# Kernel optimization log

Hardware: AMD Instinct MI355X
Metric: run time of the kernel (lower is better)

Reference implementation:

```python
import jax, jax.numpy as jnp
import numpy as np

N_SRC = 100000
N_DST = 50000
N_EDGES = 1600000
D_IN = 128
D_OUT = 64


def setup_inputs() -> dict:
    key = jax.random.key(0)
    ks = jax.random.split(key, 6)
    x = jax.random.normal(ks[0], (N_SRC, D_IN), dtype=jnp.float32)
    W_l = jax.random.normal(ks[1], (D_IN, D_OUT), dtype=jnp.float32) * (1.0 / np.sqrt(D_IN))
    b_l = jax.random.normal(ks[2], (D_OUT,), dtype=jnp.float32) * 0.01
    W_r = jax.random.normal(ks[3], (D_IN, D_OUT), dtype=jnp.float32) * (1.0 / np.sqrt(D_IN))
    src = jax.random.randint(ks[4], (N_EDGES,), 0, N_SRC, dtype=jnp.int64)
    dst = jax.random.randint(ks[5], (N_EDGES,), 0, N_DST, dtype=jnp.int64)
    edge_index = jnp.stack([src, dst], axis=0)
    return {"x": x, "W_l": W_l, "b_l": b_l, "W_r": W_r,
            "edge_index": edge_index, "n_dst": N_DST}


def reference(x, W_l, b_l, W_r, edge_index, n_dst):
    src, dst = edge_index[0], edge_index[1]
    # gather source features along edges: [E, D_in]
    msgs = x[src]
    # mean aggregation at destination nodes
    agg = jax.ops.segment_sum(msgs, dst, num_segments=n_dst)          # [n_dst, D_in]
    cnt = jax.ops.segment_sum(jnp.ones_like(dst, dtype=x.dtype), dst,
                              num_segments=n_dst)                     # [n_dst]
    mean = agg / jnp.maximum(cnt, 1.0)[:, None]
    x_target = x[:n_dst]
    # SAGEConv: lin_l(mean_agg) + lin_r(x_target)
    out = mean @ W_l + b_l + x_target @ W_r                           # [n_dst, D_out]
    return jax.nn.log_softmax(out, axis=-1)
```

## Files before the change

kernel.cpp:

```cpp
#include <hip/hip_runtime.h>
#include <math.h>

#define DIN  128
#define DOUT 64
#define PROWS 64
#define XPITCH 132
#define BSH  8
#define BMSK 255
#define BCAP 8960

__device__ inline unsigned short f2bf(float f) {
    unsigned u = __float_as_uint(f);
    u += 0x7fffu + ((u >> 16) & 1u);
    return (unsigned short)(u >> 16);
}
__device__ inline float bflo(unsigned u) { return __uint_as_float(u << 16); }
__device__ inline float bfhi(unsigned u) { return __uint_as_float(u & 0xffff0000u); }

__global__ void __launch_bounds__(256) build_k(
    const int* __restrict__ ei, unsigned* __restrict__ gTail,
    int* __restrict__ bucketBuf,
    const float* __restrict__ x, const float* __restrict__ Wl,
    const float* __restrict__ bl, const float* __restrict__ Wr,
    unsigned short* __restrict__ y, float* __restrict__ zout,
    int E, int nFill, int P, int nyb, int n_src, int n_dst, int nB)
{
    __shared__ float s_x[PROWS * XPITCH];
    const int b = blockIdx.x;
    const int fq = b / P;
    const bool isFill = ((b % P) == 0) && (fq < nFill);

    if (isFill) {
        int* s_i  = (int*)s_x;
        int* lcnt = s_i;
        int* lpos = s_i + 256;
        int* s_gb = s_i + 512;
        const int t = threadIdx.x;
        const int myb = (fq * 256 + t) * 8;
        const bool full = (myb + 8 <= E);
        int4 sa, sb4, da, db;
        if (full) {
            sa  = *(const int4*)(ei + myb);
            sb4 = *(const int4*)(ei + myb + 4);
            da  = *(const int4*)(ei + E + myb);
            db  = *(const int4*)(ei + E + myb + 4);
        }
        lcnt[t] = 0; lpos[t] = 0;
        __syncthreads();
        if (full) {
            atomicAdd(&lcnt[da.x >> BSH], 1); atomicAdd(&lcnt[da.y >> BSH], 1);
            atomicAdd(&lcnt[da.z >> BSH], 1); atomicAdd(&lcnt[da.w >> BSH], 1);
            atomicAdd(&lcnt[db.x >> BSH], 1); atomicAdd(&lcnt[db.y >> BSH], 1);
            atomicAdd(&lcnt[db.z >> BSH], 1); atomicAdd(&lcnt[db.w >> BSH], 1);
        } else {
            for (int i = myb; i < E && i < myb + 8; ++i)
                atomicAdd(&lcnt[ei[E + i] >> BSH], 1);
        }
        __syncthreads();
        if (t < nB) s_gb[t] = (int)atomicAdd(&gTail[t], (unsigned)lcnt[t]);
        __syncthreads();
#define PLACE(S, D) { int bk = (D) >> BSH; int p = atomicAdd(&lpos[bk], 1);          \
                      unsigned pos = (unsigned)(s_gb[bk] + p);                        \
                      if (pos < BCAP) bucketBuf[(size_t)bk * BCAP + pos] =            \
                          ((S) << BSH) | ((D) & BMSK); }
        if (full) {
            PLACE(sa.x,  da.x) PLACE(sa.y,  da.y) PLACE(sa.z,  da.z) PLACE(sa.w,  da.w)
            PLACE(sb4.x, db.x) PLACE(sb4.y, db.y) PLACE(sb4.z, db.z) PLACE(sb4.w, db.w)
        } else {
            for (int i = myb; i < E && i < myb + 8; ++i) {
                int s = ei[i], d = ei[E + i];
                PLACE(s, d)
            }
        }
#undef PLACE
        return;
    }

    const int fillsBefore = (fq + 1 < nFill) ? (fq + 1) : nFill;
    const int pb = b - fillsBefore;
    const int t  = threadIdx.x;
    const bool isY = (pb < nyb);
    const int rowBase = (isY ? pb : pb - nyb) * PROWS;
    const int nRows = isY ? n_src : n_dst;
    const float* __restrict__ W = isY ? Wl : Wr;

    {
        const float* xsrc = x + (size_t)rowBase * DIN;
        #pragma unroll
        for (int j = 0; j < 8; ++j) {
            int fi  = t + 256 * j;
            int row = fi >> 5, c4 = fi & 31;
            if (rowBase + row < nRows) {
                float4 v = *(const float4*)(xsrc + (size_t)fi * 4);
                *(float4*)(&s_x[row * XPITCH + c4 * 4]) = v;
            }
        }
    }
    __syncthreads();

    const int cg = t & 15;
    const int rg = t >> 4;
    const int r0 = rg * 4;
    const float* wp = W + cg * 4;

    float4 acc0 = {0.f,0.f,0.f,0.f};
    float4 acc1 = {0.f,0.f,0.f,0.f};
    float4 acc2 = {0.f,0.f,0.f,0.f};
    float4 acc3 = {0.f,0.f,0.f,0.f};

#define ROWFMA(acc, xv)                                                                     \
    acc.x = fmaf(xv.w, w3.x, fmaf(xv.z, w2.x, fmaf(xv.y, w1.x, fmaf(xv.x, w0.x, acc.x)))); \
    acc.y = fmaf(xv.w, w3.y, fmaf(xv.z, w2.y, fmaf(xv.y, w1.y, fmaf(xv.x, w0.y, acc.y)))); \
    acc.z = fmaf(xv.w, w3.z, fmaf(xv.z, w2.z, fmaf(xv.y, w1.z, fmaf(xv.x, w0.z, acc.z)))); \
    acc.w = fmaf(xv.w, w3.w, fmaf(xv.z, w2.w, fmaf(xv.y, w1.w, fmaf(xv.x, w0.w, acc.w))));

    #pragma unroll 2
    for (int k = 0; k < DIN; k += 4) {
        float4 w0 = *(const float4*)(wp + (size_t)(k + 0) * DOUT);
        float4 w1 = *(const float4*)(wp + (size_t)(k + 1) * DOUT);
        float4 w2 = *(const float4*)(wp + (size_t)(k + 2) * DOUT);
        float4 w3 = *(const float4*)(wp + (size_t)(k + 3) * DOUT);
        float4 x0 = *(const float4*)(&s_x[(r0 + 0) * XPITCH + k]);
        float4 x1 = *(const float4*)(&s_x[(r0 + 1) * XPITCH + k]);
        float4 x2 = *(const float4*)(&s_x[(r0 + 2) * XPITCH + k]);
        float4 x3 = *(const float4*)(&s_x[(r0 + 3) * XPITCH + k]);
        ROWFMA(acc0, x0)
        ROWFMA(acc1, x1)
        ROWFMA(acc2, x2)
        ROWFMA(acc3, x3)
    }
#undef ROWFMA

    if (isY) {
        float4 av[4] = {acc0, acc1, acc2, acc3};
        #pragma unroll
        for (int r = 0; r < 4; ++r) {
            int row = rowBase + r0 + r;
            if (row < nRows) {
                uint2 pk;
                pk.x = (unsigned)f2bf(av[r].x) | ((unsigned)f2bf(av[r].y) << 16);
                pk.y = (unsigned)f2bf(av[r].z) | ((unsigned)f2bf(av[r].w) << 16);
                *(uint2*)(y + (size_t)row * DOUT + cg * 4) = pk;
            }
        }
    } else {
        const float4 bv = *(const float4*)(bl + cg * 4);
        float4 av[4] = {acc0, acc1, acc2, acc3};
        #pragma unroll
        for (int r = 0; r < 4; ++r) {
            int row = rowBase + r0 + r;
            if (row < nRows) {
                float4 o;
                o.x = av[r].x + bv.x; o.y = av[r].y + bv.y;
                o.z = av[r].z + bv.z; o.w = av[r].w + bv.w;
                *(float4*)(zout + (size_t)row * DOUT + cg * 4) = o;
            }
        }
    }
}

__global__ void __launch_bounds__(256) bucket_k(
    const unsigned* __restrict__ gTail, const int* __restrict__ bucketBuf,
    int* __restrict__ rs, int* __restrict__ csr, int n_dst, int nB)
{
    __shared__ int s_ent[BCAP];
    __shared__ int s_hist[256];
    __shared__ int s_ofs[256];
    __shared__ int s_part[64];
    __shared__ int s_tails[256];
    __shared__ int s_bstart;
    const int b = blockIdx.x, t = threadIdx.x;
    const int lane = t & 63, wave = t >> 6;

    s_tails[t] = (t < nB) ? (int)gTail[t] : 0;
    s_hist[t] = 0;
    __syncthreads();
    if (t == 0) {
        int acc = 0;
        for (int j = 0; j < b; ++j) {
            int v = s_tails[j];
            acc += (v < BCAP) ? v : BCAP;
        }
        s_bstart = acc;
    }
    int m = s_tails[b]; if (m > BCAP) m = BCAP;
    __syncthreads();

    const int* bb = bucketBuf + (size_t)b * BCAP;
    for (int i = t; i < m; i += 256) {
        int e = bb[i];
        s_ent[i] = e;
        atomicAdd(&s_hist[e & BMSK], 1);
    }
    __syncthreads();

    if (t < 64) {
        s_part[t] = s_hist[4*t] + s_hist[4*t+1] + s_hist[4*t+2] + s_hist[4*t+3];
    }
    __syncthreads();
    if (wave == 0) {
        int v = s_part[lane];
        for (int o = 1; o < 64; o <<= 1) {
            int u = __shfl_up(v, o);
            if (lane >= o) v += u;
        }
        s_part[lane] = v;
    }
    __syncthreads();
    if (t < 64) {
        int base = (t == 0) ? 0 : s_part[t-1];
        int h0 = s_hist[4*t], h1 = s_hist[4*t+1], h2 = s_hist[4*t+2];
        s_ofs[4*t]   = base;
        s_ofs[4*t+1] = base + h0;
        s_ofs[4*t+2] = base + h0 + h1;
        s_ofs[4*t+3] = base + h0 + h1 + h2;
    }
    __syncthreads();

    const int dbase = b << BSH;
    int nloc = n_dst - dbase; if (nloc > 256) nloc = 256;
    const int bstart = s_bstart;
    if (t < nloc) rs[dbase + t] = bstart + s_ofs[t];
    if (t == 0)   rs[dbase + nloc] = bstart + m;
    __syncthreads();

    for (int i = t; i < m; i += 256) {
        int e = s_ent[i];
        int p = atomicAdd(&s_ofs[e & BMSK], 1);
        csr[bstart + p] = e >> BSH;
    }
}

__global__ void __launch_bounds__(256) gather_k(
    const unsigned short* __restrict__ y,
    const int* __restrict__ rs, const int* __restrict__ csr,
    float* __restrict__ out, int n_dst)
{
    const int wave = threadIdx.x >> 6, lane = threadIdx.x & 63;
    const int row = blockIdx.x * 4 + wave;
    if (row >= n_dst) return;

    const int start = rs[row];
    const int deg = rs[row + 1] - start;
    const int g = lane >> 4;
    const int qi = (lane & 15) * 2;
    const int q  = (lane & 15) * 4;
    const unsigned* yw = (const unsigned*)y;

    float4 ac0 = make_float4(0.f,0.f,0.f,0.f);
    float4 ac1 = make_float4(0.f,0.f,0.f,0.f);
    float4 ac2 = make_float4(0.f,0.f,0.f,0.f);
    float4 ac3 = make_float4(0.f,0.f,0.f,0.f);
    const int* srow = csr + start;

    for (int co = 0; co < deg; co += 64) {
        int rem = deg - co; if (rem > 64) rem = 64;
        int idx = (lane < rem) ? srow[co + lane] : 0;
        for (int i = 0; i < rem; i += 16) {
            int e0 = i + g, e1 = i + 4 + g, e2 = i + 8 + g, e3 = i + 12 + g;
            int s0 = __shfl(idx, e0), s1 = __shfl(idx, e1);
            int s2 = __shfl(idx, e2), s3 = __shfl(idx, e3);
            if (e0 < rem) { uint2 u = *(const uint2*)(yw + (size_t)s0 * 32 + qi);
                ac0.x += bflo(u.x); ac0.y += bfhi(u.x);
                ac0.z += bflo(u.y); ac0.w += bfhi(u.y); }
            if (e1 < rem) { uint2 u = *(const uint2*)(yw + (size_t)s1 * 32 + qi);
                ac1.x += bflo(u.x); ac1.y += bfhi(u.x);
                ac1.z += bflo(u.y); ac1.w += bfhi(u.y); }
            if (e2 < rem) { uint2 u = *(const uint2*)(yw + (size_t)s2 * 32 + qi);
                ac2.x += bflo(u.x); ac2.y += bfhi(u.x);
                ac2.z += bflo(u.y); ac2.w += bfhi(u.y); }
            if (e3 < rem) { uint2 u = *(const uint2*)(yw + (size_t)s3 * 32 + qi);
                ac3.x += bflo(u.x); ac3.y += bfhi(u.x);
                ac3.z += bflo(u.y); ac3.w += bfhi(u.y); }
        }
    }
    float4 acc;
    acc.x = (ac0.x + ac1.x) + (ac2.x + ac3.x);
    acc.y = (ac0.y + ac1.y) + (ac2.y + ac3.y);
    acc.z = (ac0.z + ac1.z) + (ac2.z + ac3.z);
    acc.w = (ac0.w + ac1.w) + (ac2.w + ac3.w);

    acc.x += __shfl_xor(acc.x, 32); acc.y += __shfl_xor(acc.y, 32);
    acc.z += __shfl_xor(acc.z, 32); acc.w += __shfl_xor(acc.w, 32);
    acc.x += __shfl_xor(acc.x, 16); acc.y += __shfl_xor(acc.y, 16);
    acc.z += __shfl_xor(acc.z, 16); acc.w += __shfl_xor(acc.w, 16);

    const float scale = 1.0f / (float)(deg > 0 ? deg : 1);
    const float4 zv = *(const float4*)(out + (size_t)row * DOUT + q);
    float4 v;
    v.x = acc.x * scale + zv.x;
    v.y = acc.y * scale + zv.y;
    v.z = acc.z * scale + zv.z;
    v.w = acc.w * scale + zv.w;

    float m = fmaxf(fmaxf(v.x, v.y), fmaxf(v.z, v.w));
    for (int o = 8; o >= 1; o >>= 1) m = fmaxf(m, __shfl_xor(m, o));
    float s = expf(v.x - m) + expf(v.y - m) + expf(v.z - m) + expf(v.w - m);
    for (int o = 8; o >= 1; o >>= 1) s += __shfl_xor(s, o);
    const float lse = m + logf(s);

    if (lane < 16) {
        float4 o4;
        o4.x = v.x - lse; o4.y = v.y - lse; o4.z = v.z - lse; o4.w = v.w - lse;
        *(float4*)(out + (size_t)row * DOUT + q) = o4;
    }
}

extern "C" void kernel_launch(void* const* d_in, const int* in_sizes, int n_in,
                              void* d_out, int out_size, void* d_ws, size_t ws_size,
                              hipStream_t stream)
{
    const float* x  = (const float*)d_in[0];
    const float* Wl = (const float*)d_in[1];
    const float* bl = (const float*)d_in[2];
    const float* Wr = (const float*)d_in[3];
    const int*   ei = (const int*)d_in[4];

    const int E     = in_sizes[4] / 2;
    const int n_src = in_sizes[0] / DIN;
    const int n_dst = out_size / DOUT;
    const int nB    = (n_dst + (1 << BSH) - 1) >> BSH;

    unsigned* gTail = (unsigned*)d_ws;
    int* rs  = (int*)d_ws + 256;
    int* csr = rs + (n_dst + 64);
    int* bucketBuf = csr + E;
    unsigned short* yb = (unsigned short*)(bucketBuf + (size_t)nB * BCAP);

    hipMemsetAsync(gTail, 0, 256 * sizeof(unsigned), stream);

    int nFill = (E + 2047) / 2048;
    int nyb = (n_src + PROWS - 1) / PROWS;
    int nzb = (n_dst + PROWS - 1) / PROWS;
    int total = nFill + nyb + nzb;
    int P = (total + nFill - 1) / nFill;

    build_k<<<total, 256, 0, stream>>>(
        ei, gTail, bucketBuf, x, Wl, bl, Wr, yb, (float*)d_out,
        E, nFill, P, nyb, n_src, n_dst, nB);

    bucket_k<<<nB, 256, 0, stream>>>(gTail, bucketBuf, rs, csr, n_dst, nB);

    int gG = (n_dst + 3) / 4;
    gather_k<<<gG, 256, 0, stream>>>(yb, rs, csr, (float*)d_out, n_dst);
}
```

Baseline: 225.5 us.

## Process three projection tiles per block with register-prefetched next tile

Each projection block in build_k now handles three consecutive 64-row tiles instead of one. It loads the next tile of x into registers while computing the current one, then writes those registers to shared memory between barriers. The aim is to hide global-load latency and cut block launch overhead. The cost is more registers per thread (eight float4 prefetch registers), which may lower occupancy, and fewer blocks to spread across CUs.

```diff
diff --git a/kernel.cpp b/kernel.cpp
--- a/kernel.cpp
+++ b/kernel.cpp
@@ -5,6 +5,7 @@
 #define DOUT 64
 #define PROWS 64
 #define XPITCH 132
+#define NTP  3
 #define BSH  8
 #define BMSK 255
 #define BCAP 8960
@@ -79,34 +80,63 @@
     const int fillsBefore = (fq + 1 < nFill) ? (fq + 1) : nFill;
     const int pb = b - fillsBefore;
     const int t  = threadIdx.x;
-    const bool isY = (pb < nyb);
-    const int rowBase = (isY ? pb : pb - nyb) * PROWS;
-    const int nRows = isY ? n_src : n_dst;
-    const float* __restrict__ W = isY ? Wl : Wr;
-
-    {
-        const float* xsrc = x + (size_t)rowBase * DIN;
-        #pragma unroll
-        for (int j = 0; j < 8; ++j) {
-            int fi  = t + 256 * j;
-            int row = fi >> 5, c4 = fi & 31;
-            if (rowBase + row < nRows) {
-                float4 v = *(const float4*)(xsrc + (size_t)fi * 4);
-                *(float4*)(&s_x[row * XPITCH + c4 * 4]) = v;
-            }
-        }
-    }
-    __syncthreads();
+    const int nzb = (n_dst + PROWS - 1) / PROWS;
+    const int nTiles = nyb + nzb;
+    int tt = pb * NTP;
+    if (tt >= nTiles) return;
 
     const int cg = t & 15;
     const int rg = t >> 4;
     const int r0 = rg * 4;
-    const float* wp = W + cg * 4;
-
-    float4 acc0 = {0.f,0.f,0.f,0.f};
-    float4 acc1 = {0.f,0.f,0.f,0.f};
-    float4 acc2 = {0.f,0.f,0.f,0.f};
-    float4 acc3 = {0.f,0.f,0.f,0.f};
+
+    float4 pf[8];
+    {
+        const bool isY0 = tt < nyb;
+        const int rb = (isY0 ? tt : tt - nyb) * PROWS;
+        const int nR = isY0 ? n_src : n_dst;
+        const float* xsrc = x + (size_t)rb * DIN;
+        #pragma unroll
+        for (int j = 0; j < 8; ++j) {
+            int fi = t + 256 * j;
+            int row = fi >> 5;
+            pf[j] = (rb + row < nR) ? *(const float4*)(xsrc + (size_t)fi * 4)
+                                    : make_float4(0.f, 0.f, 0.f, 0.f);
+        }
+    }
+    #pragma unroll
+    for (int j = 0; j < 8; ++j) {
+        int fi = t + 256 * j, row = fi >> 5, c4 = fi & 31;
+        *(float4*)(&s_x[row * XPITCH + c4 * 4]) = pf[j];
+    }
+    __syncthreads();
+
+    for (int i = 0; i < NTP; ++i) {
+        const int tn = tt + 1;
+        const bool hasNext = (i + 1 < NTP) && (tn < nTiles);
+        if (hasNext) {
+            const bool isYn = tn < nyb;
+            const int rb = (isYn ? tn : tn - nyb) * PROWS;
+            const int nR = isYn ? n_src : n_dst;
+            const float* xsrc = x + (size_t)rb * DIN;
+            #pragma unroll
+            for (int j = 0; j < 8; ++j) {
+                int fi = t + 256 * j;
+                int row = fi >> 5;
+                pf[j] = (rb + row < nR) ? *(const float4*)(xsrc + (size_t)fi * 4)
+                                        : make_float4(0.f, 0.f, 0.f, 0.f);
+            }
+        }
+
+        const bool isY = tt < nyb;
+        const int rowBase = (isY ? tt : tt - nyb) * PROWS;
+        const int nRows = isY ? n_src : n_dst;
+        const float* __restrict__ W = isY ? Wl : Wr;
+        const float* wp = W + cg * 4;
+
+        float4 acc0 = {0.f,0.f,0.f,0.f};
+        float4 acc1 = {0.f,0.f,0.f,0.f};
+        float4 acc2 = {0.f,0.f,0.f,0.f};
+        float4 acc3 = {0.f,0.f,0.f,0.f};
 
 #define ROWFMA(acc, xv)                                                                     \
     acc.x = fmaf(xv.w, w3.x, fmaf(xv.z, w2.x, fmaf(xv.y, w1.x, fmaf(xv.x, w0.x, acc.x)))); \
@@ -114,48 +144,59 @@
     acc.z = fmaf(xv.w, w3.z, fmaf(xv.z, w2.z, fmaf(xv.y, w1.z, fmaf(xv.x, w0.z, acc.z)))); \
     acc.w = fmaf(xv.w, w3.w, fmaf(xv.z, w2.w, fmaf(xv.y, w1.w, fmaf(xv.x, w0.w, acc.w))));
 
-    #pragma unroll 2
-    for (int k = 0; k < DIN; k += 4) {
-        float4 w0 = *(const float4*)(wp + (size_t)(k + 0) * DOUT);
-        float4 w1 = *(const float4*)(wp + (size_t)(k + 1) * DOUT);
-        float4 w2 = *(const float4*)(wp + (size_t)(k + 2) * DOUT);
-        float4 w3 = *(const float4*)(wp + (size_t)(k + 3) * DOUT);
-        float4 x0 = *(const float4*)(&s_x[(r0 + 0) * XPITCH + k]);
-        float4 x1 = *(const float4*)(&s_x[(r0 + 1) * XPITCH + k]);
-        float4 x2 = *(const float4*)(&s_x[(r0 + 2) * XPITCH + k]);
-        float4 x3 = *(const float4*)(&s_x[(r0 + 3) * XPITCH + k]);
-        ROWFMA(acc0, x0)
-        ROWFMA(acc1, x1)
-        ROWFMA(acc2, x2)
-        ROWFMA(acc3, x3)
-    }
+        #pragma unroll 2
+        for (int k = 0; k < DIN; k += 4) {
+            float4 w0 = *(const float4*)(wp + (size_t)(k + 0) * DOUT);
+            float4 w1 = *(const float4*)(wp + (size_t)(k + 1) * DOUT);
+            float4 w2 = *(const float4*)(wp + (size_t)(k + 2) * DOUT);
+            float4 w3 = *(const float4*)(wp + (size_t)(k + 3) * DOUT);
+            float4 x0 = *(const float4*)(&s_x[(r0 + 0) * XPITCH + k]);
+            float4 x1 = *(const float4*)(&s_x[(r0 + 1) * XPITCH + k]);
+            float4 x2 = *(const float4*)(&s_x[(r0 + 2) * XPITCH + k]);
+            float4 x3 = *(const float4*)(&s_x[(r0 + 3) * XPITCH + k]);
+            ROWFMA(acc0, x0)
+            ROWFMA(acc1, x1)
+            ROWFMA(acc2, x2)
+            ROWFMA(acc3, x3)
+        }
 #undef ROWFMA
 
-    if (isY) {
-        float4 av[4] = {acc0, acc1, acc2, acc3};
+        if (isY) {
+            float4 av[4] = {acc0, acc1, acc2, acc3};
+            #pragma unroll
+            for (int r = 0; r < 4; ++r) {
+                int row = rowBase + r0 + r;
+                if (row < nRows) {
+                    uint2 pk;
+                    pk.x = (unsigned)f2bf(av[r].x) | ((unsigned)f2bf(av[r].y) << 16);
+                    pk.y = (unsigned)f2bf(av[r].z) | ((unsigned)f2bf(av[r].w) << 16);
+                    *(uint2*)(y + (size_t)row * DOUT + cg * 4) = pk;
+                }
+            }
+        } else {
+            const float4 bv = *(const float4*)(bl + cg * 4);
+            float4 av[4] = {acc0, acc1, acc2, acc3};
+            #pragma unroll
+            for (int r = 0; r < 4; ++r) {
+                int row = rowBase + r0 + r;
+                if (row < nRows) {
+                    float4 o;
+                    o.x = av[r].x + bv.x; o.y = av[r].y + bv.y;
+                    o.z = av[r].z + bv.z; o.w = av[r].w + bv.w;
+                    *(float4*)(zout + (size_t)row * DOUT + cg * 4) = o;
+                }
+            }
+        }
+
+        if (!hasNext) break;
+        __syncthreads();
         #pragma unroll
-        for (int r = 0; r < 4; ++r) {
-            int row = rowBase + r0 + r;
-            if (row < nRows) {
-                uint2 pk;
-                pk.x = (unsigned)f2bf(av[r].x) | ((unsigned)f2bf(av[r].y) << 16);
-                pk.y = (unsigned)f2bf(av[r].z) | ((unsigned)f2bf(av[r].w) << 16);
-                *(uint2*)(y + (size_t)row * DOUT + cg * 4) = pk;
-            }
-        }
-    } else {
-        const float4 bv = *(const float4*)(bl + cg * 4);
-        float4 av[4] = {acc0, acc1, acc2, acc3};
-        #pragma unroll
-        for (int r = 0; r < 4; ++r) {
-            int row = rowBase + r0 + r;
-            if (row < nRows) {
-                float4 o;
-                o.x = av[r].x + bv.x; o.y = av[r].y + bv.y;
-                o.z = av[r].z + bv.z; o.w = av[r].w + bv.w;
-                *(float4*)(zout + (size_t)row * DOUT + cg * 4) = o;
-            }
-        }
+        for (int j = 0; j < 8; ++j) {
+            int fi = t + 256 * j, row = fi >> 5, c4 = fi & 31;
+            *(float4*)(&s_x[row * XPITCH + c4 * 4]) = pf[j];
+        }
+        __syncthreads();
+        tt = tn;
     }
 }
 
@@ -332,7 +373,9 @@
     int nFill = (E + 2047) / 2048;
     int nyb = (n_src + PROWS - 1) / PROWS;
     int nzb = (n_dst + PROWS - 1) / PROWS;
-    int total = nFill + nyb + nzb;
+    int nTiles = nyb + nzb;
+    int nPB = (nTiles + NTP - 1) / NTP;
+    int total = nFill + nPB;
     int P = (total + nFill - 1) / nFill;
 
     build_k<<<total, 256, 0, stream>>>(
```

Measured after the change: 261.8 us. 1.16x slower.
